# Performance work log

Hardware: AMD Instinct MI355X
Metric: run time of the kernel (lower is better)

Reference implementation:

```python
import jax, jax.numpy as jnp
import numpy as np

BLOCK_L = 32
STRIDE = 16
DIM = 128
N_DOWN = 5  # log2(BLOCK_L)


def setup_inputs() -> dict:
    key = jax.random.key(0)
    ks = jax.random.split(key, 4)
    B, H, S, D = 2, 16, 8192, DIM
    k = jax.random.normal(ks[0], (B, H, S, D), dtype=jnp.float32)
    pe = jax.random.normal(ks[1], (BLOCK_L, D), dtype=jnp.float32)
    # torch Linear weights [out, in]; down: Linear(2*dim, dim), scaled like default init
    w_down = jax.random.normal(ks[2], (N_DOWN, D, 2 * D), dtype=jnp.float32) / jnp.sqrt(2.0 * D)
    w_stop = jax.random.normal(ks[3], (D, D), dtype=jnp.float32) / jnp.sqrt(1.0 * D)
    return {"k": k, "pe": pe, "w_down": w_down, "w_stop": w_stop}


def reference(k, pe, w_down, w_stop):
    B, H, S, D = k.shape
    L = pe.shape[0]
    nb = (S - L) // STRIDE + 1  # number of sliding windows
    # unfold(-2, L, STRIDE).mT -> [B, H, nb, L, D]
    idx = STRIDE * jnp.arange(nb)[:, None] + jnp.arange(L)[None, :]  # [nb, L]
    x = k[:, :, idx, :] + pe  # broadcast pe over [B, H, nb]
    # prepend a zero block along the window axis
    x = jnp.concatenate([jnp.zeros_like(x[:, :, :1]), x], axis=2)  # [B, H, nb+1, L, D]
    # Phi: hierarchical pairwise merge, log2(L) stages
    for i in range(N_DOWN):
        Lc = x.shape[-2]
        x = x.reshape(*x.shape[:-2], Lc // 2, 2 * D)
        x = jax.nn.silu(jnp.einsum('...i,oi->...o', x, w_down[i]))
    out = jnp.einsum('...i,oi->...o', x, w_stop)  # [B, H, nb+1, 1, D]
    return out.squeeze(-2)
```

## Files before the change

kernel.cpp:

```cpp
#include <hip/hip_runtime.h>

#define BQ 2
#define HQ 16
#define SQ 8192
#define DQ 128
#define STR 16
#define NWIN 511
#define NBLK 512
#define WPB 8
#define NWG_PER_HEAD 64

typedef float f32x4 __attribute__((ext_vector_type(4)));
typedef short s16x8 __attribute__((ext_vector_type(8)));
typedef short s16x4 __attribute__((ext_vector_type(4)));

#define R_KIN  0u
#define R_S0LO 20480u
#define R_S0HI 0u
#define R_S1   20480u
#define R_S2   0u
#define R_S3   8192u
#define R_S4   12288u

static __device__ __forceinline__ unsigned swz(unsigned b) {
    return b ^ (((b >> 9) & 7u) << 4);
}

static __device__ __forceinline__ short f2bf(float f) {
    __bf16 h = (__bf16)f;
    return __builtin_bit_cast(short, h);
}

static __device__ __forceinline__ float silu(float v) {
    return v * __builtin_amdgcn_rcpf(1.f + __expf(-v));
}

__global__ void prep_kernel(const float* __restrict__ wd,
                            const float* __restrict__ wstop,
                            const float* __restrict__ pe,
                            short* __restrict__ o,
                            float* __restrict__ bias,
                            float* __restrict__ out) {
    int blk = blockIdx.x;
    if (blk < 704) {
        int i = blk * 256 + threadIdx.x;
        if (i < 163840) {
            int s   = i >> 15;
            int r   = i & 32767;
            int ct  = r >> 12;
            int r2  = r & 4095;
            int kt  = r2 >> 9;
            int r3  = r2 & 511;
            int ln  = r3 >> 3;
            int e   = r3 & 7;
            int ch  = ct * 16 + (ln & 15);
            int k   = kt * 32 + (ln >> 4) * 8 + e;
            o[i] = f2bf(wd[((size_t)(s * 128 + ch)) * 256 + k]);
        } else if (i < 180224) {
            int j   = i - 163840;
            int ct  = j >> 11;
            int r2  = j & 2047;
            int kt  = r2 >> 9;
            int r3  = r2 & 511;
            int ln  = r3 >> 3;
            int e   = r3 & 7;
            int ch  = ct * 16 + (ln & 15);
            int k   = kt * 32 + (ln >> 4) * 8 + e;
            o[i] = f2bf(wstop[ch * 128 + k]);
        }
    } else if (blk < 712) {
        int oo = (blk - 704) * 256 + threadIdx.x;
        int j = oo >> 7;
        int c = oo & 127;
        const float* w  = wd + (size_t)c * 256;
        const float* p0 = pe + (2 * j) * DQ;
        const float* p1 = pe + (2 * j + 1) * DQ;
        float s = 0.f;
        #pragma unroll 4
        for (int i = 0; i < 128; ++i) s += w[i] * p0[i];
        #pragma unroll 4
        for (int i = 0; i < 128; ++i) s += w[i + 128] * p1[i];
        bias[oo] = s;
    } else {
        int i = (blk - 712) * 256 + threadIdx.x;
        int bh = i >> 7, d = i & 127;
        out[(size_t)bh * NBLK * DQ + d] = 0.f;
    }
}

__global__ __launch_bounds__(512, 6)
void fused_kernel(const float* __restrict__ kin,
                  const short* __restrict__ wdb,
                  const float* __restrict__ bias0,
                  float* __restrict__ out) {
    __shared__ __align__(16) unsigned char lds[36864];

    const int bh = blockIdx.x >> 6;
    const int w0 = (blockIdx.x & 63) * WPB;
    const int tid  = threadIdx.x;
    const int lane = tid & 63;
    const int ct   = tid >> 6;
    const int kl   = lane >> 4;
    const int nl   = lane & 15;

    const float* kb = kin + (size_t)bh * SQ * DQ;
    const short* wbase = wdb + ct * 4096 + lane * 8;

#define LOAD_KIN(cbase) {                                                      \
        _Pragma("unroll")                                                      \
        for (int it = 0; it < 3; ++it) {                                       \
            int task = tid + it * 512;                                         \
            if (task < 1280) {                                                 \
                int rr = task >> 4;                                            \
                int c8 = task & 15;                                            \
                int srow = STR * w0 + (cbase) + rr;                            \
                if (srow > SQ - 1) srow = SQ - 1;                              \
                const float* kp = kb + (size_t)srow * DQ + c8 * 8;             \
                f32x4 a0 = *(const f32x4*)kp;                                  \
                f32x4 a1 = *(const f32x4*)(kp + 4);                            \
                s16x8 v;                                                       \
                v[0]=f2bf(a0[0]); v[1]=f2bf(a0[1]); v[2]=f2bf(a0[2]); v[3]=f2bf(a0[3]); \
                v[4]=f2bf(a1[0]); v[5]=f2bf(a1[1]); v[6]=f2bf(a1[2]); v[7]=f2bf(a1[3]); \
                *(s16x8*)(lds + swz(R_KIN + (unsigned)((rr << 8) + (c8 << 4)))) = v; \
            }                                                                  \
        } }

#define K_HALF4(W0, W1, W2, W3, P, Q, off, accv) {                             \
        s16x8 aa0 = *(const s16x8*)((P) + (off));                              \
        s16x8 aa1 = *(const s16x8*)((Q) + (off));                              \
        s16x8 aa2 = *(const s16x8*)((P) + (off) + 128);                        \
        s16x8 aa3 = *(const s16x8*)((Q) + (off) + 128);                        \
        accv = __builtin_amdgcn_mfma_f32_16x16x32_bf16(W0, aa0, accv, 0, 0, 0); \
        accv = __builtin_amdgcn_mfma_f32_16x16x32_bf16(W1, aa1, accv, 0, 0, 0); \
        accv = __builtin_amdgcn_mfma_f32_16x16x32_bf16(W2, aa2, accv, 0, 0, 0); \
        accv = __builtin_amdgcn_mfma_f32_16x16x32_bf16(W3, aa3, accv, 0, 0, 0); }

#define K_FULL(P, Q, off, accv)                                                \
        K_HALF4(wf0, wf1, wf2, wf3, P, Q, (off),       accv)                   \
        K_HALF4(wf4, wf5, wf6, wf7, P, Q, (off) + 256, accv)

#define WRITE_ROW(region, d, accv) {                                           \
        s16x4 v;                                                               \
        v[0] = f2bf(silu((accv)[0])); v[1] = f2bf(silu((accv)[1]));            \
        v[2] = f2bf(silu((accv)[2])); v[3] = f2bf(silu((accv)[3]));            \
        *(s16x4*)(lds + swz((region) + ((unsigned)(d) << 8)                    \
                            + (unsigned)(ct * 32 + kl * 8))) = v; }

#define LOAD_WF(stage_off) {                                                   \
        wf0 = *(const s16x8*)(wbase + (stage_off) + 0 * 512);                  \
        wf1 = *(const s16x8*)(wbase + (stage_off) + 1 * 512);                  \
        wf2 = *(const s16x8*)(wbase + (stage_off) + 2 * 512);                  \
        wf3 = *(const s16x8*)(wbase + (stage_off) + 3 * 512);                  \
        wf4 = *(const s16x8*)(wbase + (stage_off) + 4 * 512);                  \
        wf5 = *(const s16x8*)(wbase + (stage_off) + 5 * 512);                  \
        wf6 = *(const s16x8*)(wbase + (stage_off) + 6 * 512);                  \
        wf7 = *(const s16x8*)(wbase + (stage_off) + 7 * 512); }

    s16x8 wf0, wf1, wf2, wf3, wf4, wf5, wf6, wf7;
    LOAD_WF(0);
    const f32x4 bias = *(const f32x4*)(bias0 + nl * 128 + ct * 16 + kl * 4);

    LOAD_KIN(0);
    __syncthreads();

    const unsigned pb0 = swz(R_KIN + ((unsigned)(2 * nl) << 8) + (unsigned)(kl << 4));
    const unsigned char* P0 = lds + pb0;
    const unsigned char* Q0 = lds + (pb0 ^ 64u);

    {
        f32x4 acc0 = bias, acc1 = bias, acc2 = bias, acc3 = bias;
        K_FULL(P0, Q0, 0,     acc0);
        K_FULL(P0, Q0, 4096,  acc1);
        K_FULL(P0, Q0, 8192,  acc2);
        K_FULL(P0, Q0, 12288, acc3);
        WRITE_ROW(R_S0LO, nl,      acc0);
        WRITE_ROW(R_S0LO, 16 + nl, acc1);
        WRITE_ROW(R_S0LO, 32 + nl, acc2);
        WRITE_ROW(R_S0LO, 48 + nl, acc3);
    }
    __syncthreads();

    LOAD_KIN(64);
    __syncthreads();

    {
        f32x4 acc0 = bias, acc1 = bias, acc2 = bias, acc3 = bias;
        K_FULL(P0, Q0, 0,     acc0);
        K_FULL(P0, Q0, 4096,  acc1);
        K_FULL(P0, Q0, 8192,  acc2);
        K_FULL(P0, Q0, 12288, acc3);
        LOAD_WF(32768);
        __syncthreads();
        WRITE_ROW(R_S0HI, nl,      acc0);
        WRITE_ROW(R_S0HI, 16 + nl, acc1);
        WRITE_ROW(R_S0HI, 32 + nl, acc2);
        WRITE_ROW(R_S0HI, 48 + nl, acc3);
    }
    __syncthreads();

    {
        const unsigned plo = swz(R_S0LO + ((unsigned)(2 * nl) << 8) + (unsigned)(kl << 4));
        const unsigned char* PL = lds + plo;
        const unsigned char* QL = lds + (plo ^ 64u);
        const unsigned phi = swz(R_S0HI + ((unsigned)(2 * nl) << 8) + (unsigned)(kl << 4));
        const unsigned char* PH = lds + phi;
        const unsigned char* QH = lds + (phi ^ 64u);
        f32x4 acc0 = {}, acc1 = {}, acc2 = {}, acc3 = {};
        K_FULL(PL, QL, 0,    acc0);
        K_FULL(PL, QL, 8192, acc1);
        K_FULL(PH, QH, 0,    acc2);
        K_FULL(PH, QH, 8192, acc3);
        LOAD_WF(2 * 32768);
        __syncthreads();
        WRITE_ROW(R_S1, nl,      acc0);
        WRITE_ROW(R_S1, 16 + nl, acc1);
        WRITE_ROW(R_S1, 32 + nl, acc2);
        WRITE_ROW(R_S1, 48 + nl, acc3);
    }
    __syncthreads();

    {
        const unsigned pb = swz(R_S1 + ((unsigned)(2 * nl) << 8) + (unsigned)(kl << 4));
        const unsigned char* P = lds + pb;
        const unsigned char* Q = lds + (pb ^ 64u);
        f32x4 acc0 = {}, acc1 = {};
        K_FULL(P, Q, 0,    acc0);
        K_FULL(P, Q, 8192, acc1);
        LOAD_WF(3 * 32768);
        WRITE_ROW(R_S2, nl,      acc0);
        WRITE_ROW(R_S2, 16 + nl, acc1);
    }
    __syncthreads();

    {
        const unsigned pb = swz(R_S2 + ((unsigned)(2 * nl) << 8) + (unsigned)(kl << 4));
        const unsigned char* P = lds + pb;
        const unsigned char* Q = lds + (pb ^ 64u);
        f32x4 acc0 = {};
        K_FULL(P, Q, 0, acc0);
        LOAD_WF(4 * 32768);
        WRITE_ROW(R_S3, nl, acc0);
    }
    __syncthreads();

    {
        int dc = (nl < 8) ? nl : 7;
        const unsigned pb = swz(R_S3 + ((unsigned)(2 * dc) << 8) + (unsigned)(kl << 4));
        const unsigned char* P = lds + pb;
        const unsigned char* Q = lds + (pb ^ 64u);
        f32x4 acc0 = {};
        K_FULL(P, Q, 0, acc0);
        wf0 = *(const s16x8*)(wdb + 163840 + ct * 2048 + 0 * 512 + lane * 8);
        wf1 = *(const s16x8*)(wdb + 163840 + ct * 2048 + 1 * 512 + lane * 8);
        wf2 = *(const s16x8*)(wdb + 163840 + ct * 2048 + 2 * 512 + lane * 8);
        wf3 = *(const s16x8*)(wdb + 163840 + ct * 2048 + 3 * 512 + lane * 8);
        if (nl < 8) WRITE_ROW(R_S4, nl, acc0);
    }
    __syncthreads();

    {
        int dc = (nl < 8) ? nl : 7;
        const unsigned pb = swz(R_S4 + ((unsigned)dc << 8) + (unsigned)(kl << 4));
        const unsigned char* P = lds + pb;
        const unsigned char* Q = lds + (pb ^ 64u);
        f32x4 acc = {0.f, 0.f, 0.f, 0.f};
        K_HALF4(wf0, wf1, wf2, wf3, P, Q, 0, acc);
        int w = w0 + nl;
        if (nl < 8 && w < NWIN) {
            *(f32x4*)(out + ((size_t)bh * NBLK + (w + 1)) * DQ + ct * 16 + kl * 4) = acc;
        }
    }
#undef K_HALF4
#undef K_FULL
#undef WRITE_ROW
#undef LOAD_WF
#undef LOAD_KIN
}

extern "C" void kernel_launch(void* const* d_in, const int* in_sizes, int n_in,
                              void* d_out, int out_size, void* d_ws, size_t ws_size,
                              hipStream_t stream) {
    const float* kin   = (const float*)d_in[0];
    const float* pe    = (const float*)d_in[1];
    const float* wdown = (const float*)d_in[2];
    const float* wstop = (const float*)d_in[3];
    float* out = (float*)d_out;
    short* wbf  = (short*)d_ws;
    float* bias = (float*)((char*)d_ws + 360448);

    prep_kernel<<<728, 256, 0, stream>>>(wdown, wstop, pe, wbf, bias, out);
    fused_kernel<<<BQ * HQ * NWG_PER_HEAD, 512, 0, stream>>>(kin, wbf, bias, out);
}
```

Baseline: 77.31 us.

## Cut register pressure to raise occupancy to 8 waves per SIMD

Raises the launch bound's minimum blocks from 6 to 8 and restructures the code to lower live register counts. The bias vector is no longer held across the kernel; it is reloaded right before the stage-0 writes and added there. Accumulators are written back to LDS as soon as each is finished, and fragment loads are issued in smaller pairs. The goal is more resident waves to hide latency, at the cost of possible spills under the tighter register cap and extra bias loads.

```diff
diff --git a/kernel.cpp b/kernel.cpp
--- a/kernel.cpp
+++ b/kernel.cpp
@@ -88,7 +88,7 @@
     }
 }
 
-__global__ __launch_bounds__(512, 6)
+__global__ __launch_bounds__(512, 8)
 void fused_kernel(const float* __restrict__ kin,
                   const short* __restrict__ wdb,
                   const float* __restrict__ bias0,
@@ -125,24 +125,35 @@
             }                                                                  \
         } }
 
-#define K_HALF4(W0, W1, W2, W3, P, Q, off, accv) {                             \
-        s16x8 aa0 = *(const s16x8*)((P) + (off));                              \
-        s16x8 aa1 = *(const s16x8*)((Q) + (off));                              \
-        s16x8 aa2 = *(const s16x8*)((P) + (off) + 128);                        \
-        s16x8 aa3 = *(const s16x8*)((Q) + (off) + 128);                        \
-        accv = __builtin_amdgcn_mfma_f32_16x16x32_bf16(W0, aa0, accv, 0, 0, 0); \
-        accv = __builtin_amdgcn_mfma_f32_16x16x32_bf16(W1, aa1, accv, 0, 0, 0); \
-        accv = __builtin_amdgcn_mfma_f32_16x16x32_bf16(W2, aa2, accv, 0, 0, 0); \
-        accv = __builtin_amdgcn_mfma_f32_16x16x32_bf16(W3, aa3, accv, 0, 0, 0); }
-
-#define K_FULL(P, Q, off, accv)                                                \
-        K_HALF4(wf0, wf1, wf2, wf3, P, Q, (off),       accv)                   \
-        K_HALF4(wf4, wf5, wf6, wf7, P, Q, (off) + 256, accv)
+#define MFMA16(W, A, C) C = __builtin_amdgcn_mfma_f32_16x16x32_bf16(W, A, C, 0, 0, 0)
+
+#define K_FULL(P, Q, off, accv) {                                              \
+        { s16x8 aa0 = *(const s16x8*)((P) + (off));                            \
+          s16x8 aa1 = *(const s16x8*)((Q) + (off));                            \
+          MFMA16(wf0, aa0, accv); MFMA16(wf1, aa1, accv); }                    \
+        { s16x8 aa0 = *(const s16x8*)((P) + (off) + 128);                      \
+          s16x8 aa1 = *(const s16x8*)((Q) + (off) + 128);                      \
+          MFMA16(wf2, aa0, accv); MFMA16(wf3, aa1, accv); }                    \
+        { s16x8 aa0 = *(const s16x8*)((P) + (off) + 256);                      \
+          s16x8 aa1 = *(const s16x8*)((Q) + (off) + 256);                      \
+          MFMA16(wf4, aa0, accv); MFMA16(wf5, aa1, accv); }                    \
+        { s16x8 aa0 = *(const s16x8*)((P) + (off) + 384);                      \
+          s16x8 aa1 = *(const s16x8*)((Q) + (off) + 384);                      \
+          MFMA16(wf6, aa0, accv); MFMA16(wf7, aa1, accv); } }
 
 #define WRITE_ROW(region, d, accv) {                                           \
         s16x4 v;                                                               \
         v[0] = f2bf(silu((accv)[0])); v[1] = f2bf(silu((accv)[1]));            \
         v[2] = f2bf(silu((accv)[2])); v[3] = f2bf(silu((accv)[3]));            \
+        *(s16x4*)(lds + swz((region) + ((unsigned)(d) << 8)                    \
+                            + (unsigned)(ct * 32 + kl * 8))) = v; }
+
+#define WRITE_ROW_B(region, d, accv, bv) {                                     \
+        s16x4 v;                                                               \
+        v[0] = f2bf(silu((accv)[0] + (bv)[0]));                                \
+        v[1] = f2bf(silu((accv)[1] + (bv)[1]));                                \
+        v[2] = f2bf(silu((accv)[2] + (bv)[2]));                                \
+        v[3] = f2bf(silu((accv)[3] + (bv)[3]));                                \
         *(s16x4*)(lds + swz((region) + ((unsigned)(d) << 8)                    \
                             + (unsigned)(ct * 32 + kl * 8))) = v; }
 
@@ -158,7 +169,6 @@
 
     s16x8 wf0, wf1, wf2, wf3, wf4, wf5, wf6, wf7;
     LOAD_WF(0);
-    const f32x4 bias = *(const f32x4*)(bias0 + nl * 128 + ct * 16 + kl * 4);
 
     LOAD_KIN(0);
     __syncthreads();
@@ -168,15 +178,22 @@
     const unsigned char* Q0 = lds + (pb0 ^ 64u);
 
     {
-        f32x4 acc0 = bias, acc1 = bias, acc2 = bias, acc3 = bias;
-        K_FULL(P0, Q0, 0,     acc0);
-        K_FULL(P0, Q0, 4096,  acc1);
+        f32x4 acc0 = {}, acc1 = {};
+        K_FULL(P0, Q0, 0,    acc0);
+        K_FULL(P0, Q0, 4096, acc1);
+        {
+            const f32x4 bv = *(const f32x4*)(bias0 + nl * 128 + ct * 16 + kl * 4);
+            WRITE_ROW_B(R_S0LO, nl,      acc0, bv);
+            WRITE_ROW_B(R_S0LO, 16 + nl, acc1, bv);
+        }
+        f32x4 acc2 = {}, acc3 = {};
         K_FULL(P0, Q0, 8192,  acc2);
         K_FULL(P0, Q0, 12288, acc3);
-        WRITE_ROW(R_S0LO, nl,      acc0);
-        WRITE_ROW(R_S0LO, 16 + nl, acc1);
-        WRITE_ROW(R_S0LO, 32 + nl, acc2);
-        WRITE_ROW(R_S0LO, 48 + nl, acc3);
+        {
+            const f32x4 bv = *(const f32x4*)(bias0 + nl * 128 + ct * 16 + kl * 4);
+            WRITE_ROW_B(R_S0LO, 32 + nl, acc2, bv);
+            WRITE_ROW_B(R_S0LO, 48 + nl, acc3, bv);
+        }
     }
     __syncthreads();
 
@@ -184,17 +201,18 @@
     __syncthreads();
 
     {
-        f32x4 acc0 = bias, acc1 = bias, acc2 = bias, acc3 = bias;
+        f32x4 acc0 = {}, acc1 = {}, acc2 = {}, acc3 = {};
         K_FULL(P0, Q0, 0,     acc0);
         K_FULL(P0, Q0, 4096,  acc1);
         K_FULL(P0, Q0, 8192,  acc2);
         K_FULL(P0, Q0, 12288, acc3);
         LOAD_WF(32768);
         __syncthreads();
-        WRITE_ROW(R_S0HI, nl,      acc0);
-        WRITE_ROW(R_S0HI, 16 + nl, acc1);
-        WRITE_ROW(R_S0HI, 32 + nl, acc2);
-        WRITE_ROW(R_S0HI, 48 + nl, acc3);
+        const f32x4 bv = *(const f32x4*)(bias0 + nl * 128 + ct * 16 + kl * 4);
+        WRITE_ROW_B(R_S0HI, nl,      acc0, bv);
+        WRITE_ROW_B(R_S0HI, 16 + nl, acc1, bv);
+        WRITE_ROW_B(R_S0HI, 32 + nl, acc2, bv);
+        WRITE_ROW_B(R_S0HI, 48 + nl, acc3, bv);
     }
     __syncthreads();
 
@@ -202,18 +220,19 @@
         const unsigned plo = swz(R_S0LO + ((unsigned)(2 * nl) << 8) + (unsigned)(kl << 4));
         const unsigned char* PL = lds + plo;
         const unsigned char* QL = lds + (plo ^ 64u);
+        f32x4 acc0 = {}, acc1 = {};
+        K_FULL(PL, QL, 0,    acc0);
+        K_FULL(PL, QL, 8192, acc1);
+        __syncthreads();
+        WRITE_ROW(R_S1, nl,      acc0);
+        WRITE_ROW(R_S1, 16 + nl, acc1);
         const unsigned phi = swz(R_S0HI + ((unsigned)(2 * nl) << 8) + (unsigned)(kl << 4));
         const unsigned char* PH = lds + phi;
         const unsigned char* QH = lds + (phi ^ 64u);
-        f32x4 acc0 = {}, acc1 = {}, acc2 = {}, acc3 = {};
-        K_FULL(PL, QL, 0,    acc0);
-        K_FULL(PL, QL, 8192, acc1);
+        f32x4 acc2 = {}, acc3 = {};
         K_FULL(PH, QH, 0,    acc2);
         K_FULL(PH, QH, 8192, acc3);
         LOAD_WF(2 * 32768);
-        __syncthreads();
-        WRITE_ROW(R_S1, nl,      acc0);
-        WRITE_ROW(R_S1, 16 + nl, acc1);
         WRITE_ROW(R_S1, 32 + nl, acc2);
         WRITE_ROW(R_S1, 48 + nl, acc3);
     }
@@ -223,11 +242,12 @@
         const unsigned pb = swz(R_S1 + ((unsigned)(2 * nl) << 8) + (unsigned)(kl << 4));
         const unsigned char* P = lds + pb;
         const unsigned char* Q = lds + (pb ^ 64u);
-        f32x4 acc0 = {}, acc1 = {};
-        K_FULL(P, Q, 0,    acc0);
+        f32x4 acc0 = {};
+        K_FULL(P, Q, 0, acc0);
+        WRITE_ROW(R_S2, nl, acc0);
+        f32x4 acc1 = {};
         K_FULL(P, Q, 8192, acc1);
         LOAD_WF(3 * 32768);
-        WRITE_ROW(R_S2, nl,      acc0);
         WRITE_ROW(R_S2, 16 + nl, acc1);
     }
     __syncthreads();
@@ -264,15 +284,21 @@
         const unsigned char* P = lds + pb;
         const unsigned char* Q = lds + (pb ^ 64u);
         f32x4 acc = {0.f, 0.f, 0.f, 0.f};
-        K_HALF4(wf0, wf1, wf2, wf3, P, Q, 0, acc);
+        { s16x8 aa0 = *(const s16x8*)(P);
+          s16x8 aa1 = *(const s16x8*)(Q);
+          MFMA16(wf0, aa0, acc); MFMA16(wf1, aa1, acc); }
+        { s16x8 aa0 = *(const s16x8*)(P + 128);
+          s16x8 aa1 = *(const s16x8*)(Q + 128);
+          MFMA16(wf2, aa0, acc); MFMA16(wf3, aa1, acc); }
         int w = w0 + nl;
         if (nl < 8 && w < NWIN) {
             *(f32x4*)(out + ((size_t)bh * NBLK + (w + 1)) * DQ + ct * 16 + kl * 4) = acc;
         }
     }
-#undef K_HALF4
+#undef MFMA16
 #undef K_FULL
 #undef WRITE_ROW
+#undef WRITE_ROW_B
 #undef LOAD_WF
 #undef LOAD_KIN
 }
```

Result: slower. 91.66 us (+18.6%).
